# Kernel tuning notes

Hardware: AMD Instinct MI355X
Metric: run time of the kernel (lower is better)

Reference implementation:

```python
import jax, jax.numpy as jnp
import numpy as np

B, T, W, D = 16, 32, 128, 1024  # batch, turns, words/turn, hidden dim


def setup_inputs() -> dict:
    key = jax.random.key(0)
    ks = jax.random.split(key, 6)
    source = jax.random.normal(ks[0], (B, 1, D), dtype=jnp.float32)
    memory_bank = jax.random.normal(ks[1], (B, T, W, D), dtype=jnp.float32)
    # lengths in [1, W] so no turn is fully masked (matches real padded batches)
    memory_lengths = jax.random.randint(ks[2], (B, T), 1, W + 1)
    memory_turns = jax.random.randint(ks[3], (B,), 1, T + 1)
    # nn.Linear(indim, outdim, bias=False): y = x @ W^T; store as [indim, outdim]
    W_word = jax.random.normal(ks[4], (D, D), dtype=jnp.float32) * 0.02
    W_turn = jax.random.normal(ks[5], (D, D), dtype=jnp.float32) * 0.02
    return {"source": source, "memory_bank": memory_bank,
            "memory_lengths": memory_lengths, "memory_turns": memory_turns,
            "W_word": W_word, "W_turn": W_turn}


def reference(source, memory_bank, memory_lengths, memory_turns, W_word, W_turn):
    # source: [B,1,D]; memory_bank: [B,T,W,D]; target_l == 1
    b, t, w, d = memory_bank.shape
    # ---- word-level attention (per turn) ----
    q_w = source @ W_word                                   # [B,1,D]
    word_scores = jnp.einsum('bqd,btwd->btw', q_w, memory_bank)  # [B,T,W]
    word_mask = jnp.arange(w)[None, None, :] < memory_lengths[:, :, None]
    word_scores = jnp.where(word_mask, word_scores, -jnp.inf)
    word_attn = jax.nn.softmax(word_scores, axis=-1)        # [B,T,W]
    # zero out fully-padded turns (length == 0)
    word_attn = word_attn * (memory_lengths > 0)[:, :, None].astype(word_attn.dtype)
    cw = jnp.einsum('btw,btwd->btd', word_attn, memory_bank)  # [B,T,D]
    # ---- turn-level attention ----
    q_t = source @ W_turn                                   # [B,1,D]
    turn_scores = jnp.einsum('bqd,btd->bt', q_t, cw)        # [B,T]
    turn_mask = jnp.arange(t)[None, :] < memory_turns[:, None]
    turn_scores = jnp.where(turn_mask, turn_scores, -jnp.inf)
    turn_attn = jax.nn.softmax(turn_scores, axis=-1)        # [B,T]
    ct = jnp.einsum('bt,btd->bd', turn_attn, cw)            # [B,D]
    return ct
```

## Files before the change

### kernel.cpp

```cpp
#include <hip/hip_runtime.h>
#include <math.h>

#define Bn 16
#define Tn 32
#define Wn 128
#define Dn 1024


__global__ __launch_bounds__(256) void qproj_kernel(
    const float* __restrict__ src, const float* __restrict__ Ww,
    const float* __restrict__ Wt, float* __restrict__ qwp, float* __restrict__ qtp)
{
    __shared__ float s_lds[16 * 520];
    const int tid = threadIdx.x;
    const int mat = blockIdx.x >> 5;
    const int chunk = (blockIdx.x >> 1) & 15;
    const int isl = blockIdx.x & 1;

    for (int k = 0; k < 32; ++k) {
        int idx = k * 256 + tid;
        int bb = idx >> 9, ii = idx & 511;
        s_lds[bb * 520 + ii] = src[bb * 1024 + isl * 512 + ii];
    }
    __syncthreads();

    const int lane = tid & 63, wv = tid >> 6;
    const int col4 = chunk * 16 + (lane & 15);
    const int b = (lane >> 4) + 4 * wv;
    const float4* W4 = (const float4*)(mat ? Wt : Ww);
    const float* sb = s_lds + b * 520;

    float4 acc = make_float4(0.f, 0.f, 0.f, 0.f);
    #pragma unroll 8
    for (int ii = 0; ii < 512; ++ii) {
        int i = isl * 512 + ii;
        float4 w4 = W4[i * 256 + col4];
        float s = sb[ii];
        acc.x = fmaf(s, w4.x, acc.x);
        acc.y = fmaf(s, w4.y, acc.y);
        acc.z = fmaf(s, w4.z, acc.z);
        acc.w = fmaf(s, w4.w, acc.w);
    }
    float* qo = (mat ? qtp : qwp) + isl * (Bn * Dn);
    ((float4*)(qo + b * Dn))[col4] = acc;
}

__global__ __launch_bounds__(512) void word_attn_kernel(
    const float* __restrict__ mem, const float* __restrict__ qwp,
    const float* __restrict__ qtp, const int* __restrict__ lens,
    const int* __restrict__ turns, float* __restrict__ cw, float* __restrict__ ts)
{
    const int bt = blockIdx.x;
    const int b = bt >> 5, t = bt & 31;
    if (t >= turns[b]) return;
    const int len = lens[bt];

    const int tid = threadIdx.x, lane = tid & 63, wv = tid >> 6;
    const float* rowb = mem + (size_t)bt * (Wn * Dn);

    const float4* qa = (const float4*)(qwp + b * Dn);
    const float4* qb = (const float4*)(qwp + Bn * Dn + b * Dn);
    float4 q[4];
    #pragma unroll
    for (int c = 0; c < 4; ++c) {
        float4 a = qa[c * 64 + lane], bb = qb[c * 64 + lane];
        q[c] = make_float4(a.x + bb.x, a.y + bb.y, a.z + bb.z, a.w + bb.w);
    }

    float m = -INFINITY, l = 0.f;
    float4 acc[4];
    #pragma unroll
    for (int c = 0; c < 4; ++c) acc[c] = make_float4(0.f, 0.f, 0.f, 0.f);

    for (int w = wv; w < len; w += 8) {
        const float4* r4 = (const float4*)(rowb + (size_t)w * Dn);
        float4 x[4];
        #pragma unroll
        for (int c = 0; c < 4; ++c) x[c] = r4[c * 64 + lane];
        float s = 0.f;
        #pragma unroll
        for (int c = 0; c < 4; ++c) {
            s = fmaf(q[c].x, x[c].x, s);
            s = fmaf(q[c].y, x[c].y, s);
            s = fmaf(q[c].z, x[c].z, s);
            s = fmaf(q[c].w, x[c].w, s);
        }
        #pragma unroll
        for (int off = 32; off >= 1; off >>= 1) s += __shfl_xor(s, off, 64);

        float mn = fmaxf(m, s);
        float sc = (m == -INFINITY) ? 0.f : __expf(m - mn);
        float p = __expf(s - mn);
        l = l * sc + p;
        #pragma unroll
        for (int c = 0; c < 4; ++c) {
            acc[c].x = fmaf(acc[c].x, sc, p * x[c].x);
            acc[c].y = fmaf(acc[c].y, sc, p * x[c].y);
            acc[c].z = fmaf(acc[c].z, sc, p * x[c].z);
            acc[c].w = fmaf(acc[c].w, sc, p * x[c].w);
        }
        m = mn;
    }

    __shared__ float m_s[8], l_s[8], red[8];
    __shared__ float acc_s[8 * 1024];
    if (lane == 0) { m_s[wv] = m; l_s[wv] = l; }
    float4* as4 = (float4*)(acc_s + wv * 1024);
    #pragma unroll
    for (int c = 0; c < 4; ++c) as4[c * 64 + lane] = acc[c];
    __syncthreads();

    float M = -INFINITY;
    #pragma unroll
    for (int v = 0; v < 8; ++v) M = fmaxf(M, m_s[v]);
    float L = 0.f, cx = 0.f, cy = 0.f;
    const float2* a2 = (const float2*)acc_s;
    #pragma unroll
    for (int v = 0; v < 8; ++v) {
        float f = (l_s[v] > 0.f) ? __expf(m_s[v] - M) : 0.f;
        L += f * l_s[v];
        float2 a = a2[v * 512 + tid];
        cx = fmaf(f, a.x, cx);
        cy = fmaf(f, a.y, cy);
    }
    float inv = 1.f / L;
    cx *= inv; cy *= inv;
    ((float2*)(cw + (size_t)bt * Dn))[tid] = make_float2(cx, cy);

    const float2* qta = (const float2*)(qtp + b * Dn);
    const float2* qtb = (const float2*)(qtp + Bn * Dn + b * Dn);
    float2 t0 = qta[tid], t1 = qtb[tid];
    float p = (t0.x + t1.x) * cx + (t0.y + t1.y) * cy;
    #pragma unroll
    for (int off = 32; off >= 1; off >>= 1) p += __shfl_xor(p, off, 64);
    if (lane == 0) red[wv] = p;
    __syncthreads();
    if (tid == 0) {
        float r = 0.f;
        #pragma unroll
        for (int v = 0; v < 8; ++v) r += red[v];
        ts[bt] = r;
    }
}

__global__ __launch_bounds__(256) void turn_attn_kernel(
    const float* __restrict__ cw, const float* __restrict__ ts,
    const int* __restrict__ turns, float* __restrict__ out)
{
    const int b = blockIdx.x;
    const int n = turns[b];
    const int tid = threadIdx.x;
    __shared__ float attn[32];
    if (tid < 32) {
        float s = (tid < n) ? ts[b * Tn + tid] : -INFINITY;
        float mm = s;
        #pragma unroll
        for (int off = 16; off >= 1; off >>= 1) mm = fmaxf(mm, __shfl_xor(mm, off, 32));
        float e = (tid < n) ? __expf(s - mm) : 0.f;
        float sum = e;
        #pragma unroll
        for (int off = 16; off >= 1; off >>= 1) sum += __shfl_xor(sum, off, 32);
        attn[tid] = e / sum;
    }
    __syncthreads();
    float4 a = make_float4(0.f, 0.f, 0.f, 0.f);
    for (int tt = 0; tt < n; ++tt) {
        float wgt = attn[tt];
        float4 c = ((const float4*)(cw + ((size_t)b * Tn + tt) * Dn))[tid];
        a.x = fmaf(wgt, c.x, a.x);
        a.y = fmaf(wgt, c.y, a.y);
        a.z = fmaf(wgt, c.z, a.z);
        a.w = fmaf(wgt, c.w, a.w);
    }
    ((float4*)(out + b * Dn))[tid] = a;
}

extern "C" void kernel_launch(void* const* d_in, const int* in_sizes, int n_in,
                              void* d_out, int out_size, void* d_ws, size_t ws_size,
                              hipStream_t stream) {
    (void)in_sizes; (void)n_in; (void)out_size; (void)ws_size;
    const float* src   = (const float*)d_in[0];
    const float* mem   = (const float*)d_in[1];
    const int*   lens  = (const int*)d_in[2];
    const int*   turns = (const int*)d_in[3];
    const float* Ww    = (const float*)d_in[4];
    const float* Wt    = (const float*)d_in[5];
    float* ws  = (float*)d_ws;
    float* qwp = ws;
    float* qtp = ws + 2 * Bn * Dn;
    float* cw  = ws + 4 * Bn * Dn;
    float* ts  = cw + (size_t)Bn * Tn * Dn;
    float* out = (float*)d_out;

    hipLaunchKernelGGL(qproj_kernel, dim3(64), dim3(256), 0, stream,
                       src, Ww, Wt, qwp, qtp);
    hipLaunchKernelGGL(word_attn_kernel, dim3(Bn * Tn), dim3(512), 0, stream,
                       mem, qwp, qtp, lens, turns, cw, ts);
    hipLaunchKernelGGL(turn_attn_kernel, dim3(Bn), dim3(256), 0, stream,
                       cw, ts, turns, out);
}
```

Measured before the change: 373.4 us.

## Split query projection eight ways with reduce kernel; widen word attention to 1024 threads

The query projection now splits the reduction dimension into 8 slices over 256 blocks instead of 2 slices over 64, which gives more parallelism for streaming the weight matrices. A new small kernel sums the partial results into final q vectors. The word-attention kernel moves from 512 to 1024 threads (16 waves per block), giving more memory-level parallelism per block when streaming the memory bank. The cost is an extra kernel launch, a larger LDS footprint (64KB) per block, and possibly lower block-level occupancy.

```diff
diff --git a/kernel.cpp b/kernel.cpp
--- a/kernel.cpp
+++ b/kernel.cpp
@@ -11,16 +11,17 @@
     const float* __restrict__ src, const float* __restrict__ Ww,
     const float* __restrict__ Wt, float* __restrict__ qwp, float* __restrict__ qtp)
 {
-    __shared__ float s_lds[16 * 520];
+    __shared__ float s_lds[16 * 132];
     const int tid = threadIdx.x;
-    const int mat = blockIdx.x >> 5;
-    const int chunk = (blockIdx.x >> 1) & 15;
-    const int isl = blockIdx.x & 1;
-
-    for (int k = 0; k < 32; ++k) {
+    const int mat = blockIdx.x >> 7;
+    const int chunk = (blockIdx.x >> 3) & 15;
+    const int isl = blockIdx.x & 7;
+
+    #pragma unroll
+    for (int k = 0; k < 8; ++k) {
         int idx = k * 256 + tid;
-        int bb = idx >> 9, ii = idx & 511;
-        s_lds[bb * 520 + ii] = src[bb * 1024 + isl * 512 + ii];
+        int bb = idx >> 7, ii = idx & 127;
+        s_lds[bb * 132 + ii] = src[bb * Dn + isl * 128 + ii];
     }
     __syncthreads();
 
@@ -28,13 +29,12 @@
     const int col4 = chunk * 16 + (lane & 15);
     const int b = (lane >> 4) + 4 * wv;
     const float4* W4 = (const float4*)(mat ? Wt : Ww);
-    const float* sb = s_lds + b * 520;
+    const float* sb = s_lds + b * 132;
 
     float4 acc = make_float4(0.f, 0.f, 0.f, 0.f);
     #pragma unroll 8
-    for (int ii = 0; ii < 512; ++ii) {
-        int i = isl * 512 + ii;
-        float4 w4 = W4[i * 256 + col4];
+    for (int ii = 0; ii < 128; ++ii) {
+        float4 w4 = W4[(size_t)(isl * 128 + ii) * 256 + col4];
         float s = sb[ii];
         acc.x = fmaf(s, w4.x, acc.x);
         acc.y = fmaf(s, w4.y, acc.y);
@@ -45,9 +45,26 @@
     ((float4*)(qo + b * Dn))[col4] = acc;
 }
 
-__global__ __launch_bounds__(512) void word_attn_kernel(
-    const float* __restrict__ mem, const float* __restrict__ qwp,
-    const float* __restrict__ qtp, const int* __restrict__ lens,
+__global__ __launch_bounds__(256) void qreduce_kernel(
+    const float* __restrict__ qwp, const float* __restrict__ qtp,
+    float* __restrict__ qw, float* __restrict__ qt)
+{
+    const int blk = blockIdx.x;
+    const float4* in4 = (const float4*)((blk & 16) ? qtp : qwp);
+    float4* out4 = (float4*)((blk & 16) ? qt : qw);
+    const int idx = (blk & 15) * 256 + threadIdx.x;
+    float4 a = make_float4(0.f, 0.f, 0.f, 0.f);
+    #pragma unroll
+    for (int s = 0; s < 8; ++s) {
+        float4 v = in4[s * 4096 + idx];
+        a.x += v.x; a.y += v.y; a.z += v.z; a.w += v.w;
+    }
+    out4[idx] = a;
+}
+
+__global__ __launch_bounds__(1024) void word_attn_kernel(
+    const float* __restrict__ mem, const float* __restrict__ qw,
+    const float* __restrict__ qt, const int* __restrict__ lens,
     const int* __restrict__ turns, float* __restrict__ cw, float* __restrict__ ts)
 {
     const int bt = blockIdx.x;
@@ -58,21 +75,17 @@
     const int tid = threadIdx.x, lane = tid & 63, wv = tid >> 6;
     const float* rowb = mem + (size_t)bt * (Wn * Dn);
 
-    const float4* qa = (const float4*)(qwp + b * Dn);
-    const float4* qb = (const float4*)(qwp + Bn * Dn + b * Dn);
+    const float4* qa = (const float4*)(qw + b * Dn);
     float4 q[4];
     #pragma unroll
-    for (int c = 0; c < 4; ++c) {
-        float4 a = qa[c * 64 + lane], bb = qb[c * 64 + lane];
-        q[c] = make_float4(a.x + bb.x, a.y + bb.y, a.z + bb.z, a.w + bb.w);
-    }
+    for (int c = 0; c < 4; ++c) q[c] = qa[c * 64 + lane];
 
     float m = -INFINITY, l = 0.f;
     float4 acc[4];
     #pragma unroll
     for (int c = 0; c < 4; ++c) acc[c] = make_float4(0.f, 0.f, 0.f, 0.f);
 
-    for (int w = wv; w < len; w += 8) {
+    for (int w = wv; w < len; w += 16) {
         const float4* r4 = (const float4*)(rowb + (size_t)w * Dn);
         float4 x[4];
         #pragma unroll
@@ -102,8 +115,8 @@
         m = mn;
     }
 
-    __shared__ float m_s[8], l_s[8], red[8];
-    __shared__ float acc_s[8 * 1024];
+    __shared__ float m_s[16], l_s[16], red[16];
+    __shared__ float acc_s[16 * 1024];
     if (lane == 0) { m_s[wv] = m; l_s[wv] = l; }
     float4* as4 = (float4*)(acc_s + wv * 1024);
     #pragma unroll
@@ -112,25 +125,18 @@
 
     float M = -INFINITY;
     #pragma unroll
-    for (int v = 0; v < 8; ++v) M = fmaxf(M, m_s[v]);
-    float L = 0.f, cx = 0.f, cy = 0.f;
-    const float2* a2 = (const float2*)acc_s;
-    #pragma unroll
-    for (int v = 0; v < 8; ++v) {
+    for (int v = 0; v < 16; ++v) M = fmaxf(M, m_s[v]);
+    float L = 0.f, cacc = 0.f;
+    #pragma unroll
+    for (int v = 0; v < 16; ++v) {
         float f = (l_s[v] > 0.f) ? __expf(m_s[v] - M) : 0.f;
         L += f * l_s[v];
-        float2 a = a2[v * 512 + tid];
-        cx = fmaf(f, a.x, cx);
-        cy = fmaf(f, a.y, cy);
-    }
-    float inv = 1.f / L;
-    cx *= inv; cy *= inv;
-    ((float2*)(cw + (size_t)bt * Dn))[tid] = make_float2(cx, cy);
-
-    const float2* qta = (const float2*)(qtp + b * Dn);
-    const float2* qtb = (const float2*)(qtp + Bn * Dn + b * Dn);
-    float2 t0 = qta[tid], t1 = qtb[tid];
-    float p = (t0.x + t1.x) * cx + (t0.y + t1.y) * cy;
+        cacc = fmaf(f, acc_s[v * 1024 + tid], cacc);
+    }
+    cacc *= 1.f / L;
+    cw[(size_t)bt * Dn + tid] = cacc;
+
+    float p = qt[b * Dn + tid] * cacc;
     #pragma unroll
     for (int off = 32; off >= 1; off >>= 1) p += __shfl_xor(p, off, 64);
     if (lane == 0) red[wv] = p;
@@ -138,7 +144,7 @@
     if (tid == 0) {
         float r = 0.f;
         #pragma unroll
-        for (int v = 0; v < 8; ++v) r += red[v];
+        for (int v = 0; v < 16; ++v) r += red[v];
         ts[bt] = r;
     }
 }
@@ -187,15 +193,19 @@
     const float* Wt    = (const float*)d_in[5];
     float* ws  = (float*)d_ws;
     float* qwp = ws;
-    float* qtp = ws + 2 * Bn * Dn;
-    float* cw  = ws + 4 * Bn * Dn;
+    float* qtp = ws + 8 * Bn * Dn;
+    float* qw  = ws + 16 * Bn * Dn;
+    float* qt  = ws + 17 * Bn * Dn;
+    float* cw  = ws + 18 * Bn * Dn;
     float* ts  = cw + (size_t)Bn * Tn * Dn;
     float* out = (float*)d_out;
 
-    hipLaunchKernelGGL(qproj_kernel, dim3(64), dim3(256), 0, stream,
+    hipLaunchKernelGGL(qproj_kernel, dim3(256), dim3(256), 0, stream,
                        src, Ww, Wt, qwp, qtp);
-    hipLaunchKernelGGL(word_attn_kernel, dim3(Bn * Tn), dim3(512), 0, stream,
-                       mem, qwp, qtp, lens, turns, cw, ts);
+    hipLaunchKernelGGL(qreduce_kernel, dim3(32), dim3(256), 0, stream,
+                       qwp, qtp, qw, qt);
+    hipLaunchKernelGGL(word_attn_kernel, dim3(Bn * Tn), dim3(1024), 0, stream,
+                       mem, qw, qt, lens, turns, cw, ts);
     hipLaunchKernelGGL(turn_attn_kernel, dim3(Bn), dim3(256), 0, stream,
                        cw, ts, turns, out);
 }
```

Result: faster. 351.8 us (-5.8%).
